# Kernel optimization log

Hardware: AMD Instinct MI355X
Metric: run time of the kernel (lower is better)

The kernel has to match this reference:

```python
import jax, jax.numpy as jnp
import numpy as np

# Straight-through sign binarization: forward -> {-1, +1}, backward -> identity
@jax.custom_vjp
def binarize(x):
    return jnp.where(x >= 0, jnp.ones_like(x), -jnp.ones_like(x))

def _bin_fwd(x):
    return binarize(x), None

def _bin_bwd(res, g):
    return (g,)

binarize.defvjp(_bin_fwd, _bin_bwd)

BATCH = 16384
IN_SIZE = 1025   # must be 2**n + 1
HIDDEN = 1025    # must be 2**n + 1

def setup_inputs() -> dict:
    key = jax.random.key(0)
    k0, k1, k2, k3 = jax.random.split(key, 4)
    # weight init scale per reset_parameters: sqrt(1.5/(in+out)) uniform
    s = float(np.sqrt(1.5 / (IN_SIZE + HIDDEN)))
    return {
        "x": jax.random.normal(k0, (BATCH, IN_SIZE), dtype=jnp.float32),
        "W0": jax.random.uniform(k1, (HIDDEN, IN_SIZE), jnp.float32, -s, s),
        "W1": jax.random.uniform(k2, (HIDDEN, HIDDEN), jnp.float32, -s, s),
        "W2": jax.random.uniform(k3, (1, HIDDEN), jnp.float32, -s, s),
    }

def reference(x, W0, W1, W2):
    # x: [B, IN_SIZE]; weights stored [out, in] (nn.Linear convention), no bias
    h = x.reshape(-1, IN_SIZE)
    for W in (W0, W1, W2):
        lin = h @ binarize(W).T          # float GEMM against +/-1 weights
        h = binarize(lin)                # sign activation
    # num_classes == 2 path: to_boolean maps {-1,+1} -> {0,1}, then squeeze
    out = (h + 1.0) * 0.5
    return out.squeeze(-1)               # [B]
```

## Files before the change

### kernel.cpp

```cpp
#include <hip/hip_runtime.h>
#include <cstdint>

typedef unsigned long long u64;
typedef unsigned short ushort_t;
typedef __attribute__((ext_vector_type(8))) short short8;
typedef __attribute__((ext_vector_type(4))) float f32x4;

#define B_TOTAL 16384
#define K_DIM   1025
#define O_DIM   1025
#define NWORDS  17
#define NKT     34
#define NFRAG   72
#define A_BYTES 8192
#define B_BYTES 73728
#define STEP_BYTES (A_BYTES + B_BYTES)
#define FLAG_CAP 4096
#define L23_ROWS 16

__device__ __forceinline__ ushort_t f2bf_rne(float f) {
  unsigned u = __float_as_uint(f);
  return (ushort_t)((u + 0x7fffu + ((u >> 16) & 1u)) >> 16);
}

__device__ __forceinline__ void gload16(const ushort_t* g, char* l) {
  __builtin_amdgcn_global_load_lds(
      (const __attribute__((address_space(1))) void*)g,
      (__attribute__((address_space(3))) void*)l, 16, 0, 0);
}

__global__ __launch_bounds__(256) void pack_all_kernel(const float* __restrict__ W0,
                                                       const float* __restrict__ W1,
                                                       const float* __restrict__ W2,
                                                       u64* __restrict__ w0b,
                                                       u64* __restrict__ w1b,
                                                       u64* __restrict__ w2b) {
  __shared__ unsigned char by[136];
  const int row = blockIdx.x, t = threadIdx.x;
  const float* src; u64* dst; int o;
  if (row < O_DIM)           { src = W0; dst = w0b; o = row; }
  else if (row < 2 * O_DIM)  { src = W1; dst = w1b; o = row - O_DIM; }
  else                       { src = W2; dst = w2b; o = 0; }
  if (t < 136) {
    const float* wr = src + (size_t)o * K_DIM;
    unsigned m = 0;
#pragma unroll
    for (int j = 0; j < 8; ++j) {
      int k = t * 8 + j;
      bool pos = (k < K_DIM) ? (wr[k] >= 0.0f) : true;
      m |= (unsigned)pos << j;
    }
    by[t] = (unsigned char)m;
  }
  __syncthreads();
  if (t < NWORDS) {
    u64 word = 0;
#pragma unroll
    for (int q = 0; q < 8; ++q) word |= (u64)by[t * 8 + q] << (8 * q);
    dst[(size_t)o * NWORDS + t] = word;
  }
}

__global__ __launch_bounds__(256) void prep_sbf_kernel(const float* __restrict__ w0,
                                                       ushort_t* __restrict__ sbf) {
  const int t = threadIdx.x;
  const int f = blockIdx.x * 4 + (t >> 6);
  const int lane = t & 63;
  const int kt = f / NFRAG, nf = f % NFRAG;
  const int o = nf * 16 + (lane & 15);
  const int kbase = kt * 32 + (lane >> 4) * 8;
  short8 sv;
#pragma unroll
  for (int j = 0; j < 8; ++j) {
    int k = kbase + j;
    short v = 0;
    if (o < O_DIM && k < K_DIM)
      v = (short)((w0[(size_t)o * K_DIM + k] >= 0.0f) ? 0x3F80 : 0xBF80);
    sv[j] = v;
  }
  *(short8*)&sbf[(size_t)f * 512 + lane * 8] = sv;
}

__global__ __launch_bounds__(512, 2) void l1_fused_kernel(
    const ushort_t* __restrict__ sbf, const float* __restrict__ x,
    const u64* __restrict__ w0b, u64* __restrict__ h1b) {
  extern __shared__ char smem[];
  const int p = blockIdx.x;
  const int t = threadIdx.x;
  const int wave = t >> 6, lane = t & 63;
  const int lr = lane & 15, lg = lane >> 4;
  const int b0 = p * 64;
  const int obase = wave * 144;

  const int u = t & 255;
  const int cmf = u >> 6, clane = u & 63;
  const int crow = cmf * 16 + (clane & 15);
  const int ckb0 = (clane >> 4) * 8;
  const bool isLo = (t >= 256);
  const float* xrowC = x + (size_t)(b0 + crow) * K_DIM;
  const int convOff = (isLo ? 4096 : 0) + cmf * 1024 + clane * 16;

  f32x4 acc[4][9];
#pragma unroll
  for (int mf = 0; mf < 4; ++mf)
#pragma unroll
    for (int nfl = 0; nfl < 9; ++nfl)
#pragma unroll
      for (int c = 0; c < 4; ++c) acc[mf][nfl][c] = 0.0f;

  float xv[8];
  float sAcc = 0.0f;

#define LOADX(KT)                                                              \
  {                                                                            \
    int kb = (KT) * 32 + ckb0;                                                 \
    const float* xr = xrowC + kb;                                              \
    if (kb + 8 <= K_DIM) {                                                     \
      float4 a = *(const float4*)xr;                                           \
      float4 b = *(const float4*)(xr + 4);                                     \
      xv[0]=a.x; xv[1]=a.y; xv[2]=a.z; xv[3]=a.w;                              \
      xv[4]=b.x; xv[5]=b.y; xv[6]=b.z; xv[7]=b.w;                              \
    } else {                                                                   \
      _Pragma("unroll")                                                        \
      for (int j = 0; j < 8; ++j) xv[j] = (kb + j < K_DIM) ? xr[j] : 0.0f;     \
    }                                                                          \
  }

#define CONVERT_WRITE(DBUF)                                                    \
  {                                                                            \
    short8 w8;                                                                 \
    if (!isLo) {                                                               \
      _Pragma("unroll")                                                        \
      for (int j = 0; j < 8; ++j) {                                            \
        float v = xv[j];                                                       \
        sAcc += fabsf(v);                                                      \
        w8[j] = (short)f2bf_rne(v);                                            \
      }                                                                        \
    } else {                                                                   \
      _Pragma("unroll")                                                        \
      for (int j = 0; j < 8; ++j) {                                            \
        float v = xv[j];                                                       \
        ushort_t h = f2bf_rne(v);                                              \
        float hf = __uint_as_float((unsigned)h << 16);                         \
        w8[j] = (short)f2bf_rne(v - hf);                                       \
      }                                                                        \
    }                                                                          \
    *(short8*)((DBUF) + convOff) = w8;                                         \
  }

#define GLOADB(KT, DBUF)                                                       \
  {                                                                            \
    _Pragma("unroll")                                                          \
    for (int i = 0; i < 9; ++i) {                                              \
      int sfr = wave * 9 + i;                                                  \
      gload16(sbf + (size_t)(KT) * (B_BYTES / 2) + sfr * 512 + lane * 8,       \
              (DBUF) + A_BYTES + sfr * 1024);                                  \
    }                                                                          \
  }

  LOADX(0); CONVERT_WRITE(smem);
  GLOADB(0, smem);
  __syncthreads();

  int cur = 0;
  for (int kt = 0; kt < NKT; ++kt) {
    char* nbuf = smem + (cur ^ 1) * STEP_BYTES;
    if (kt + 1 < NKT) {
      LOADX(kt + 1);
      GLOADB(kt + 1, nbuf);
    }
    const ushort_t* A = (const ushort_t*)(smem + cur * STEP_BYTES);
    const ushort_t* Bf = A + A_BYTES / 2;
    short8 ah[4], al[4];
#pragma unroll
    for (int mf = 0; mf < 4; ++mf) {
      ah[mf] = *(const short8*)&A[mf * 512 + lane * 8];
      al[mf] = *(const short8*)&A[(4 + mf) * 512 + lane * 8];
    }
#pragma unroll
    for (int nfl = 0; nfl < 9; ++nfl) {
      short8 bv = *(const short8*)&Bf[(wave * 9 + nfl) * 512 + lane * 8];
#pragma unroll
      for (int mf = 0; mf < 4; ++mf) {
        acc[mf][nfl] = __builtin_amdgcn_mfma_f32_16x16x32_bf16(ah[mf], bv, acc[mf][nfl], 0, 0, 0);
        acc[mf][nfl] = __builtin_amdgcn_mfma_f32_16x16x32_bf16(al[mf], bv, acc[mf][nfl], 0, 0, 0);
      }
    }
    if (kt + 1 < NKT) CONVERT_WRITE(nbuf);
    __syncthreads();
    cur ^= 1;
  }
#undef LOADX
#undef CONVERT_WRITE
#undef GLOADB

  unsigned char* bits = (unsigned char*)smem;
  u64*      hs    = (u64*)(smem + 73728);
  unsigned* list  = (unsigned*)(smem + 82432);
  unsigned* lcnt  = (unsigned*)(smem + 98816);
  float*    errbL = (float*)(smem + 98832);
  unsigned* hsw   = (unsigned*)hs;

  sAcc += __shfl_xor(sAcc, 16, 64);
  sAcc += __shfl_xor(sAcc, 32, 64);
  if (t == 0) *lcnt = 0;
  if (!isLo && lg == 0)
    errbL[crow] = sAcc * (1.02f / 65536.0f) + 0.125f;
  __syncthreads();

  float eb[4][4];
#pragma unroll
  for (int mf = 0; mf < 4; ++mf)
#pragma unroll
    for (int rg = 0; rg < 4; ++rg) eb[mf][rg] = errbL[mf * 16 + lg * 4 + rg];

#pragma unroll
  for (int mf = 0; mf < 4; ++mf)
#pragma unroll
    for (int nfl = 0; nfl < 9; ++nfl)
#pragma unroll
      for (int rg = 0; rg < 4; ++rg) {
        int bl = mf * 16 + lg * 4 + rg;
        int o  = obase + nfl * 16 + lr;
        float lin = acc[mf][nfl][rg];
        unsigned abit = (lin >= 0.0f) ? 1u : 0u;
        bits[bl * 1152 + o] = (unsigned char)abit;
        if ((o < O_DIM) && (fabsf(lin) <= eb[mf][rg])) {
          unsigned idx = atomicAdd(lcnt, 1u);
          if (idx < FLAG_CAP)
            list[idx] = ((unsigned)bl << 12) | ((unsigned)o << 1) | abit;
        }
      }
  __syncthreads();

  for (int task = t; task < 64 * NWORDS; task += 512) {
    int row = task / NWORDS, w = task % NWORDS;
    u64 word = 0;
#pragma unroll
    for (int q = 0; q < 8; ++q) {
      u64 v = *(const u64*)&bits[row * 1152 + w * 64 + q * 8];
#pragma unroll
      for (int m = 0; m < 8; ++m)
        word |= ((v >> (8 * m)) & 1ull) << (q * 8 + m);
    }
    int rem = O_DIM - w * 64;
    if (rem < 64) word |= (~0ull << rem);
    hs[row * NWORDS + w] = word;
  }
  __syncthreads();

  {
    unsigned n = *lcnt; if (n > FLAG_CAP) n = FLAG_CAP;
    for (unsigned i = t; i < n; i += 512) {
      unsigned en = list[i];
      int bl = (int)(en >> 12), o = (int)((en >> 1) & 0x7ffu);
      unsigned abit = en & 1u;
      const float* xr = x + (size_t)(b0 + bl) * K_DIM;
      const u64* wr = w0b + (size_t)o * NWORDS;
      float a = 0.0f;
      for (int j = 0; j < 16; ++j) {
        u64 wd = wr[j];
#pragma unroll
        for (int m = 0; m < 64; ++m) {
          float v = xr[j * 64 + m];
          unsigned neg = ((unsigned)(wd >> m) & 1u) ^ 1u;
          a += __uint_as_float(__float_as_uint(v) ^ (neg << 31));
        }
      }
      {
        u64 wd = wr[16];
        float v = xr[1024];
        unsigned neg = ((unsigned)wd & 1u) ^ 1u;
        a += __uint_as_float(__float_as_uint(v) ^ (neg << 31));
      }
      unsigned nb = (a >= 0.0f) ? 1u : 0u;
      if (nb != abit)
        atomicXor(&hsw[bl * 34 + (o >> 5)], 1u << (o & 31));
    }
  }
  __syncthreads();

  for (int task = t; task < 64 * NWORDS; task += 512)
    h1b[(size_t)b0 * NWORDS + task] = hs[task];
}

__global__ __launch_bounds__(256) void l2l3_kernel(const u64* __restrict__ h1b,
                                                   const u64* __restrict__ w1b,
                                                   const u64* __restrict__ w2b,
                                                   float* __restrict__ out) {
  __shared__ u64 hs[L23_ROWS][NWORDS];
  __shared__ u64 h2[L23_ROWS][NWORDS];
  const int bt = blockIdx.x;
  const int t = threadIdx.x;
  for (int i = t; i < L23_ROWS * NWORDS; i += 256)
    hs[i / NWORDS][i % NWORDS] = h1b[(size_t)(bt * L23_ROWS + i / NWORDS) * NWORDS + i % NWORDS];
  __syncthreads();

  const int w = t >> 6, l = t & 63;
  for (int oc = w; oc < NWORDS; oc += 4) {
    int o = oc * 64 + l;
    bool valid = (o < O_DIM);
    int orow = valid ? o : (O_DIM - 1);
    u64 wb[NWORDS];
#pragma unroll
    for (int j = 0; j < NWORDS; ++j) wb[j] = w1b[(size_t)orow * NWORDS + j];
    for (int b = 0; b < L23_ROWS; b += 2) {
      int p0 = 0, p1 = 0;
#pragma unroll
      for (int j = 0; j < NWORDS; ++j) {
        p0 += __popcll(hs[b + 0][j] ^ wb[j]);
        p1 += __popcll(hs[b + 1][j] ^ wb[j]);
      }
      u64 m0 = __ballot(valid ? (K_DIM - 2 * p0 >= 0) : true);
      u64 m1 = __ballot(valid ? (K_DIM - 2 * p1 >= 0) : true);
      if (l == 0) h2[b + 0][oc] = m0;
      if (l == 1) h2[b + 1][oc] = m1;
    }
  }
  __syncthreads();
  if (t < L23_ROWS) {
    int p = 0;
#pragma unroll
    for (int j = 0; j < NWORDS; ++j) p += __popcll(h2[t][j] ^ w2b[j]);
    out[bt * L23_ROWS + t] = ((K_DIM - 2 * p) >= 0) ? 1.0f : 0.0f;
  }
}

extern "C" void kernel_launch(void* const* d_in, const int* in_sizes, int n_in,
                              void* d_out, int out_size, void* d_ws, size_t ws_size,
                              hipStream_t stream) {
  const float* x  = (const float*)d_in[0];
  const float* W0 = (const float*)d_in[1];
  const float* W1 = (const float*)d_in[2];
  const float* W2 = (const float*)d_in[3];
  float* out = (float*)d_out;

  char* ws = (char*)d_ws;
  u64*      w0b  = (u64*)(ws);
  u64*      w1b  = (u64*)(ws + 139776);
  u64*      w2b  = (u64*)(ws + 279552);
  u64*      h1b  = (u64*)(ws + 280064);
  ushort_t* sbf  = (ushort_t*)(ws + 2508288);

  static bool attr_set = false;
  if (!attr_set) {
    hipFuncSetAttribute((const void*)l1_fused_kernel,
                        hipFuncAttributeMaxDynamicSharedMemorySize, 2 * STEP_BYTES);
    attr_set = true;
  }

  pack_all_kernel<<<2 * O_DIM + 1, 256, 0, stream>>>(W0, W1, W2, w0b, w1b, w2b);
  prep_sbf_kernel<<<NKT * NFRAG / 4, 256, 0, stream>>>(W0, sbf);
  l1_fused_kernel<<<B_TOTAL / 64, 512, 2 * STEP_BYTES, stream>>>(sbf, x, w0b, h1b);
  l2l3_kernel<<<B_TOTAL / L23_ROWS, 256, 0, stream>>>(h1b, w1b, w2b, out);
}
```

Before: 165.0 us.

## Load weight fragments directly into registers instead of staging through LDS

The layer-1 GEMM no longer stages the pre-swizzled bf16 weight fragments through shared memory with global_load_lds. Each wave now loads its own 9 B fragments straight into registers, double-buffered across two register sets, and the k-loop is unrolled by two. Only the small activation tile stays in LDS, so the dynamic shared memory request drops from about 160 KB to about 97 KB, which may allow more blocks per CU and removes the LDS reads of B. In exchange, register pressure rises by 18 short8 values per thread, which could reduce occupancy or cause spills.

```diff
diff --git a/kernel.cpp b/kernel.cpp
--- a/kernel.cpp
+++ b/kernel.cpp
@@ -14,19 +14,13 @@
 #define NFRAG   72
 #define A_BYTES 8192
 #define B_BYTES 73728
-#define STEP_BYTES (A_BYTES + B_BYTES)
+#define SMEM_BYTES 99328
 #define FLAG_CAP 4096
 #define L23_ROWS 16
 
 __device__ __forceinline__ ushort_t f2bf_rne(float f) {
   unsigned u = __float_as_uint(f);
   return (ushort_t)((u + 0x7fffu + ((u >> 16) & 1u)) >> 16);
-}
-
-__device__ __forceinline__ void gload16(const ushort_t* g, char* l) {
-  __builtin_amdgcn_global_load_lds(
-      (const __attribute__((address_space(1))) void*)g,
-      (__attribute__((address_space(3))) void*)l, 16, 0, 0);
 }
 
 __global__ __launch_bounds__(256) void pack_all_kernel(const float* __restrict__ W0,
@@ -100,6 +94,8 @@
   const float* xrowC = x + (size_t)(b0 + crow) * K_DIM;
   const int convOff = (isLo ? 4096 : 0) + cmf * 1024 + clane * 16;
 
+  const ushort_t* gB = sbf + (size_t)(wave * 9) * 512 + lane * 8;
+
   f32x4 acc[4][9];
 #pragma unroll
   for (int mf = 0; mf < 4; ++mf)
@@ -110,6 +106,7 @@
 
   float xv[8];
   float sAcc = 0.0f;
+  short8 bX[9], bY[9];
 
 #define LOADX(KT)                                                              \
   {                                                                            \
@@ -148,51 +145,55 @@
     *(short8*)((DBUF) + convOff) = w8;                                         \
   }
 
-#define GLOADB(KT, DBUF)                                                       \
+#define LOADB(REG, KT)                                                         \
   {                                                                            \
     _Pragma("unroll")                                                          \
-    for (int i = 0; i < 9; ++i) {                                              \
-      int sfr = wave * 9 + i;                                                  \
-      gload16(sbf + (size_t)(KT) * (B_BYTES / 2) + sfr * 512 + lane * 8,       \
-              (DBUF) + A_BYTES + sfr * 1024);                                  \
+    for (int i = 0; i < 9; ++i)                                                \
+      (REG)[i] = *(const short8*)&gB[(size_t)(KT) * (B_BYTES / 2) + i * 512];  \
+  }
+
+#define MFMA_STEP(AOFF, BREG)                                                  \
+  {                                                                            \
+    const ushort_t* A = (const ushort_t*)(smem + (AOFF));                      \
+    short8 ah[4], al[4];                                                       \
+    _Pragma("unroll")                                                          \
+    for (int mf = 0; mf < 4; ++mf) {                                           \
+      ah[mf] = *(const short8*)&A[mf * 512 + lane * 8];                        \
+      al[mf] = *(const short8*)&A[(4 + mf) * 512 + lane * 8];                  \
     }                                                                          \
+    _Pragma("unroll")                                                          \
+    for (int nfl = 0; nfl < 9; ++nfl) {                                        \
+      _Pragma("unroll")                                                        \
+      for (int mf = 0; mf < 4; ++mf) {                                         \
+        acc[mf][nfl] = __builtin_amdgcn_mfma_f32_16x16x32_bf16(ah[mf], (BREG)[nfl], acc[mf][nfl], 0, 0, 0); \
+        acc[mf][nfl] = __builtin_amdgcn_mfma_f32_16x16x32_bf16(al[mf], (BREG)[nfl], acc[mf][nfl], 0, 0, 0); \
+      }                                                                        \
+    }                                                                          \
   }
 
   LOADX(0); CONVERT_WRITE(smem);
-  GLOADB(0, smem);
-  __syncthreads();
-
-  int cur = 0;
-  for (int kt = 0; kt < NKT; ++kt) {
-    char* nbuf = smem + (cur ^ 1) * STEP_BYTES;
-    if (kt + 1 < NKT) {
+  LOADB(bX, 0);
+  __syncthreads();
+
+  for (int kt = 0; kt < NKT; kt += 2) {
+    {
+      LOADB(bY, kt + 1);
       LOADX(kt + 1);
-      GLOADB(kt + 1, nbuf);
-    }
-    const ushort_t* A = (const ushort_t*)(smem + cur * STEP_BYTES);
-    const ushort_t* Bf = A + A_BYTES / 2;
-    short8 ah[4], al[4];
-#pragma unroll
-    for (int mf = 0; mf < 4; ++mf) {
-      ah[mf] = *(const short8*)&A[mf * 512 + lane * 8];
-      al[mf] = *(const short8*)&A[(4 + mf) * 512 + lane * 8];
-    }
-#pragma unroll
-    for (int nfl = 0; nfl < 9; ++nfl) {
-      short8 bv = *(const short8*)&Bf[(wave * 9 + nfl) * 512 + lane * 8];
-#pragma unroll
-      for (int mf = 0; mf < 4; ++mf) {
-        acc[mf][nfl] = __builtin_amdgcn_mfma_f32_16x16x32_bf16(ah[mf], bv, acc[mf][nfl], 0, 0, 0);
-        acc[mf][nfl] = __builtin_amdgcn_mfma_f32_16x16x32_bf16(al[mf], bv, acc[mf][nfl], 0, 0, 0);
-      }
-    }
-    if (kt + 1 < NKT) CONVERT_WRITE(nbuf);
-    __syncthreads();
-    cur ^= 1;
+      MFMA_STEP(0, bX);
+      CONVERT_WRITE(smem + 8192);
+      __syncthreads();
+    }
+    {
+      if (kt + 2 < NKT) { LOADB(bX, kt + 2); LOADX(kt + 2); }
+      MFMA_STEP(8192, bY);
+      if (kt + 2 < NKT) CONVERT_WRITE(smem + 0);
+      __syncthreads();
+    }
   }
 #undef LOADX
 #undef CONVERT_WRITE
-#undef GLOADB
+#undef LOADB
+#undef MFMA_STEP
 
   unsigned char* bits = (unsigned char*)smem;
   u64*      hs    = (u64*)(smem + 73728);
@@ -345,12 +346,12 @@
   static bool attr_set = false;
   if (!attr_set) {
     hipFuncSetAttribute((const void*)l1_fused_kernel,
-                        hipFuncAttributeMaxDynamicSharedMemorySize, 2 * STEP_BYTES);
+                        hipFuncAttributeMaxDynamicSharedMemorySize, SMEM_BYTES);
     attr_set = true;
   }
 
   pack_all_kernel<<<2 * O_DIM + 1, 256, 0, stream>>>(W0, W1, W2, w0b, w1b, w2b);
   prep_sbf_kernel<<<NKT * NFRAG / 4, 256, 0, stream>>>(W0, sbf);
-  l1_fused_kernel<<<B_TOTAL / 64, 512, 2 * STEP_BYTES, stream>>>(sbf, x, w0b, h1b);
+  l1_fused_kernel<<<B_TOTAL / 64, 512, SMEM_BYTES, stream>>>(sbf, x, w0b, h1b);
   l2l3_kernel<<<B_TOTAL / L23_ROWS, 256, 0, stream>>>(h1b, w1b, w2b, out);
 }
```

After: 219.9 us. 1.33x slower.
